# Performance work log

Measured on AMD Instinct MI355X. Metric: run time of the kernel, lower is better.

Reference implementation:

```python
import jax, jax.numpy as jnp
import numpy as np
from jax import lax

BN_EPS = 1e-5
K = 2  # kernel_size


def setup_inputs() -> dict:
    key = jax.random.key(0)
    k1, k2, k3 = jax.random.split(key, 3)
    x = jax.random.normal(k1, (64, 3, 256, 256), dtype=jnp.float32)
    conv_w = jax.random.normal(k2, (16, 3, K, K), dtype=jnp.float32) * 0.1
    conv_b = jax.random.normal(k3, (16,), dtype=jnp.float32) * 0.1
    gamma = jnp.ones((16,), dtype=jnp.float32)
    beta = jnp.zeros((16,), dtype=jnp.float32)
    return {"x": x, "conv_w": conv_w, "conv_b": conv_b, "gamma": gamma, "beta": beta}


def _forward(x, conv_w, conv_b, gamma, beta):
    # Conv2d, stride 1, VALID padding -> [B, C, H, W]
    feat = lax.conv_general_dilated(
        x, conv_w, window_strides=(1, 1), padding="VALID",
        dimension_numbers=("NCHW", "OIHW", "NCHW"))
    feat = feat + conv_b[None, :, None, None]
    # BatchNorm2d in training mode: batch stats over (B, H, W) per channel
    mu = jnp.mean(feat, axis=(0, 2, 3), keepdims=True)
    var = jnp.var(feat, axis=(0, 2, 3), keepdims=True)
    feat = (feat - mu) * lax.rsqrt(var + BN_EPS)
    feat = feat * gamma[None, :, None, None] + beta[None, :, None, None]
    feat = jax.nn.relu(feat)
    # Default quantum filter: mean(tanh(window)) over [C, k, k] window at every (b, i, j)
    t = jnp.tanh(feat)
    C = t.shape[1]
    win_sum = lax.reduce_window(
        t, jnp.float32(0), lax.add,
        window_dimensions=(1, C, K, K), window_strides=(1, 1, 1, 1),
        padding="VALID")  # [B, 1, H-k+1, W-k+1]
    out = win_sum / (C * K * K)
    # Flatten in (b, i, j) order, matching the triple loop
    return out.reshape(-1)


def reference(x, conv_w, conv_b, gamma, beta):
    return _forward(x, conv_w, conv_b, gamma, beta)
```

## Files before the change

kernel.cpp:

```cpp
#include <hip/hip_runtime.h>

#define B     64
#define CIN   3
#define COUT  16
#define H     256
#define W     256
#define HW    (H*W)
#define CHW   (CIN*H*W)
#define HO    255
#define WO    255
#define HF    254
#define WF    254
#define NPIXF 4161600.0f
#define BN_EPS 1e-5f
#define C2TANH 2.8853900817779268f

#define SEGS  32
#define NITEM (B * HO * SEGS)
#define STB   (NITEM / 256)

#define RB    7
#define RBLKS 37
#define LSTR  260

__device__ __forceinline__ float4 ld4(const float* p) { return *(const float4*)p; }

__device__ __forceinline__ void load_patch(const float* xp, int off8,
                                           float x0[CIN][9], float x1[CIN][9]) {
#pragma unroll
    for (int ic = 0; ic < CIN; ic++) {
        const float* p0 = xp + ic * HW;
        const float* p1 = p0 + W;
        float4 a = ld4(p0), b = ld4(p0 + 4);
        x0[ic][0] = a.x; x0[ic][1] = a.y; x0[ic][2] = a.z; x0[ic][3] = a.w;
        x0[ic][4] = b.x; x0[ic][5] = b.y; x0[ic][6] = b.z; x0[ic][7] = b.w;
        x0[ic][8] = p0[off8];
        float4 c4 = ld4(p1), d = ld4(p1 + 4);
        x1[ic][0] = c4.x; x1[ic][1] = c4.y; x1[ic][2] = c4.z; x1[ic][3] = c4.w;
        x1[ic][4] = d.x;  x1[ic][5] = d.y;  x1[ic][6] = d.z;  x1[ic][7] = d.w;
        x1[ic][8] = p1[off8];
    }
}

#define CONV_F(u)                                                  \
    float f = wd.x;                                                \
    f = fmaf(wa.x, x0[0][u], f); f = fmaf(wa.y, x0[0][(u)+1], f);  \
    f = fmaf(wa.z, x1[0][u], f); f = fmaf(wa.w, x1[0][(u)+1], f);  \
    f = fmaf(wb.x, x0[1][u], f); f = fmaf(wb.y, x0[1][(u)+1], f);  \
    f = fmaf(wb.z, x1[1][u], f); f = fmaf(wb.w, x1[1][(u)+1], f);  \
    f = fmaf(wc4.x, x0[2][u], f); f = fmaf(wc4.y, x0[2][(u)+1], f);\
    f = fmaf(wc4.z, x1[2][u], f); f = fmaf(wc4.w, x1[2][(u)+1], f);

__global__ __launch_bounds__(256) void k_stats(const float* __restrict__ x,
                                               const float* __restrict__ w,
                                               const float* __restrict__ bias,
                                               float* __restrict__ acc) {
    __shared__ float wpk[COUT * 16];
    int tid = threadIdx.x;
    {
        int c = tid >> 4, k = tid & 15;
        float v = 0.f;
        if (k < 12)       v = w[c * 12 + k];
        else if (k == 12) v = bias[c];
        wpk[tid] = v;
    }
    __syncthreads();

    int item = blockIdx.x * 256 + tid;
    int jseg = item & (SEGS - 1);
    int row  = item >> 5;
    int bb   = row / HO;
    int i    = row - bb * HO;
    const float* xp = x + (size_t)bb * CHW + i * W + (jseg << 3);
    bool tail = (jseg == SEGS - 1);
    int  off8 = tail ? 7 : 8;
    float m7  = tail ? 0.f : 1.f;

    float x0[CIN][9], x1[CIN][9];
    load_patch(xp, off8, x0, x1);

    float s[COUT], q[COUT];
#pragma unroll
    for (int c = 0; c < COUT; c++) {
        const float4* wv = (const float4*)(wpk + (c << 4));
        float4 wa = wv[0], wb = wv[1], wc4 = wv[2], wd = wv[3];
        float sc_ = 0.f, qc_ = 0.f;
#pragma unroll
        for (int u = 0; u < 8; u++) {
            CONV_F(u)
            if (u == 7) f *= m7;
            sc_ += f;
            qc_ = fmaf(f, f, qc_);
        }
        s[c] = sc_;
        q[c] = qc_;
    }

#pragma unroll
    for (int c = 0; c < COUT; c++) {
        for (int off = 32; off; off >>= 1) {
            s[c] += __shfl_down(s[c], off, 64);
            q[c] += __shfl_down(q[c], off, 64);
        }
    }
    __shared__ float red[4][2 * COUT];
    int wave = tid >> 6, lane = tid & 63;
    if (lane == 0) {
#pragma unroll
        for (int c = 0; c < COUT; c++) {
            red[wave][c] = s[c];
            red[wave][COUT + c] = q[c];
        }
    }
    __syncthreads();
    if (tid < 2 * COUT) {
        float v = red[0][tid] + red[1][tid] + red[2][tid] + red[3][tid];
        atomicAdd(&acc[tid], v);
    }
}

__global__ __launch_bounds__(256) void k_csum(const float* __restrict__ x,
                                              const float* __restrict__ w,
                                              const float* __restrict__ bias,
                                              const float* __restrict__ gamma,
                                              const float* __restrict__ beta,
                                              const float* __restrict__ acc,
                                              float* __restrict__ out) {
    __shared__ float wpk[COUT * 16];
    __shared__ float sld[(RB + 1) * LSTR];
    int tid = threadIdx.x;
    {
        int c = tid >> 4, k = tid & 15;
        float v = 0.f;
        if (k < 12)       v = w[c * 12 + k];
        else if (k == 12) v = bias[c];
        else if (k < 15) {
            float sv = acc[c], qv = acc[COUT + c];
            float mu  = sv * (1.f / NPIXF);
            float var = qv * (1.f / NPIXF) - mu * mu;
            float sc  = gamma[c] * rsqrtf(var + BN_EPS);
            v = (k == 13) ? sc * C2TANH : (beta[c] - mu * sc) * C2TANH;
        }
        wpk[tid] = v;
    }
    int blk   = blockIdx.x;
    int bb    = blk / RBLKS;
    int rblk  = blk - bb * RBLKS;
    int rbase = rblk * RB;
    __syncthreads();

    int sr = tid >> 5;
    int si = rbase + sr;
    int jseg = tid & 31;
    int j0 = jseg << 3;
    if (si < HO) {
        const float* xp = x + (size_t)bb * CHW + si * W + j0;
        int off8 = (jseg == 31) ? 7 : 8;
        float x0[CIN][9], x1[CIN][9];
        load_patch(xp, off8, x0, x1);

        float sum[8];
#pragma unroll
        for (int u = 0; u < 8; u++) sum[u] = 0.f;

#pragma unroll
        for (int c = 0; c < COUT; c++) {
            const float4* wv4 = (const float4*)(wpk + (c << 4));
            float4 wa = wv4[0], wb = wv4[1], wc4 = wv4[2], wd = wv4[3];
#pragma unroll
            for (int u = 0; u < 8; u++) {
                CONV_F(u)
                float a2 = fmaf(wd.y, f, wd.z);
                a2 = fmaxf(a2, 0.f);
                float E = __builtin_amdgcn_exp2f(a2);
                float r = __builtin_amdgcn_rcpf(E + 1.f);
                sum[u] += r;
            }
        }
        float* sp = &sld[sr * LSTR + j0];
        *(float4*)sp       = make_float4(fmaf(-2.f, sum[0], (float)COUT),
                                         fmaf(-2.f, sum[1], (float)COUT),
                                         fmaf(-2.f, sum[2], (float)COUT),
                                         fmaf(-2.f, sum[3], (float)COUT));
        *(float4*)(sp + 4) = make_float4(fmaf(-2.f, sum[4], (float)COUT),
                                         fmaf(-2.f, sum[5], (float)COUT),
                                         fmaf(-2.f, sum[6], (float)COUT),
                                         fmaf(-2.f, sum[7], (float)COUT));
    }
    __syncthreads();

    int orl = tid >> 5;
    int orow = rbase + orl;
    if (orl < RB && orow < HF) {
        const float* s0 = &sld[orl * LSTR];
        const float* s1 = s0 + LSTR;
        float* op = out + ((size_t)bb * HF + orow) * WF;
        int oc0 = tid & 31;
#pragma unroll
        for (int u = 0; u < 8; u++) {
            int c = oc0 + (u << 5);
            if (c < WF) {
                op[c] = (s0[c] + s0[c+1] + s1[c] + s1[c+1]) * (1.f / (COUT * 4));
            }
        }
    }
}

extern "C" void kernel_launch(void* const* d_in, const int* in_sizes, int n_in,
                              void* d_out, int out_size, void* d_ws, size_t ws_size,
                              hipStream_t stream) {
    const float* x     = (const float*)d_in[0];
    const float* w     = (const float*)d_in[1];
    const float* bias  = (const float*)d_in[2];
    const float* gamma = (const float*)d_in[3];
    const float* beta  = (const float*)d_in[4];
    float* out = (float*)d_out;

    float* acc = (float*)d_ws;

    hipMemsetAsync(d_ws, 0, 128, stream);
    k_stats<<<STB, 256, 0, stream>>>(x, w, bias, acc);
    k_csum<<<B * RBLKS, 256, 0, stream>>>(x, w, bias, gamma, beta, acc, out);
}
```

Measured before the change: 182.1 us.

## Replace atomic stats accumulation with per-block partials and a reduce kernel

k_stats now writes per-block sums into a partials buffer instead of doing global atomicAdds. The block reduction switches from wave shuffles to a transposed shared-memory reduction. A new single-block kernel sums the partials into the accumulator, which also removes the memset. This aims to cut atomic contention and shuffle cost, and makes the sum order deterministic. The trade-offs are an extra launch, a serial single-block reduce over about 4080 rows, and much more shared memory per block, which may lower occupancy.

```diff
diff --git a/kernel.cpp b/kernel.cpp
--- a/kernel.cpp
+++ b/kernel.cpp
@@ -18,6 +18,7 @@
 #define SEGS  32
 #define NITEM (B * HO * SEGS)
 #define STB   (NITEM / 256)
+#define RCHUNK (STB / 8)
 
 #define RB    7
 #define RBLKS 37
@@ -54,8 +55,10 @@
 __global__ __launch_bounds__(256) void k_stats(const float* __restrict__ x,
                                                const float* __restrict__ w,
                                                const float* __restrict__ bias,
-                                               float* __restrict__ acc) {
+                                               float* __restrict__ part) {
     __shared__ float wpk[COUT * 16];
+    __shared__ float tr[256 * 33];
+    __shared__ float red2[8 * 33];
     int tid = threadIdx.x;
     {
         int c = tid >> 4, k = tid & 15;
@@ -79,7 +82,6 @@
     float x0[CIN][9], x1[CIN][9];
     load_patch(xp, off8, x0, x1);
 
-    float s[COUT], q[COUT];
 #pragma unroll
     for (int c = 0; c < COUT; c++) {
         const float4* wv = (const float4*)(wpk + (c << 4));
@@ -92,30 +94,55 @@
             sc_ += f;
             qc_ = fmaf(f, f, qc_);
         }
-        s[c] = sc_;
-        q[c] = qc_;
-    }
-
-#pragma unroll
-    for (int c = 0; c < COUT; c++) {
-        for (int off = 32; off; off >>= 1) {
-            s[c] += __shfl_down(s[c], off, 64);
-            q[c] += __shfl_down(q[c], off, 64);
-        }
-    }
-    __shared__ float red[4][2 * COUT];
-    int wave = tid >> 6, lane = tid & 63;
-    if (lane == 0) {
-#pragma unroll
-        for (int c = 0; c < COUT; c++) {
-            red[wave][c] = s[c];
-            red[wave][COUT + c] = q[c];
-        }
-    }
-    __syncthreads();
-    if (tid < 2 * COUT) {
-        float v = red[0][tid] + red[1][tid] + red[2][tid] + red[3][tid];
-        atomicAdd(&acc[tid], v);
+        tr[tid * 33 + c]        = sc_;
+        tr[tid * 33 + COUT + c] = qc_;
+    }
+    __syncthreads();
+
+    {
+        int col = tid & 31, chunk = tid >> 5;
+        int r0 = chunk << 5;
+        float a0 = 0.f, a1 = 0.f, a2 = 0.f, a3 = 0.f;
+#pragma unroll
+        for (int k = 0; k < 32; k += 4) {
+            a0 += tr[(r0 + k)     * 33 + col];
+            a1 += tr[(r0 + k + 1) * 33 + col];
+            a2 += tr[(r0 + k + 2) * 33 + col];
+            a3 += tr[(r0 + k + 3) * 33 + col];
+        }
+        red2[chunk * 33 + col] = (a0 + a1) + (a2 + a3);
+    }
+    __syncthreads();
+    if (tid < 32) {
+        float s = 0.f;
+#pragma unroll
+        for (int k = 0; k < 8; k++) s += red2[k * 33 + tid];
+        part[blockIdx.x * 32 + tid] = s;
+    }
+}
+
+__global__ __launch_bounds__(256) void k_reduce(const float* __restrict__ part,
+                                                float* __restrict__ acc) {
+    __shared__ float red2[8 * 33];
+    int tid = threadIdx.x;
+    int col = tid & 31, chunk = tid >> 5;
+    int base = chunk * RCHUNK;
+    float a0 = 0.f, a1 = 0.f, a2 = 0.f, a3 = 0.f;
+    int k = 0;
+    for (; k + 3 < RCHUNK; k += 4) {
+        a0 += part[(base + k)     * 32 + col];
+        a1 += part[(base + k + 1) * 32 + col];
+        a2 += part[(base + k + 2) * 32 + col];
+        a3 += part[(base + k + 3) * 32 + col];
+    }
+    for (; k < RCHUNK; k++) a0 += part[(base + k) * 32 + col];
+    red2[chunk * 33 + col] = (a0 + a1) + (a2 + a3);
+    __syncthreads();
+    if (tid < 32) {
+        float s = 0.f;
+#pragma unroll
+        for (int j = 0; j < 8; j++) s += red2[j * 33 + tid];
+        acc[tid] = s;
     }
 }
 
@@ -216,9 +243,10 @@
     const float* beta  = (const float*)d_in[4];
     float* out = (float*)d_out;
 
-    float* acc = (float*)d_ws;
-
-    hipMemsetAsync(d_ws, 0, 128, stream);
-    k_stats<<<STB, 256, 0, stream>>>(x, w, bias, acc);
+    float* part = (float*)d_ws;
+    float* acc  = part + STB * 32;
+
+    k_stats<<<STB, 256, 0, stream>>>(x, w, bias, part);
+    k_reduce<<<1, 256, 0, stream>>>(part, acc);
     k_csum<<<B * RBLKS, 256, 0, stream>>>(x, w, bias, gamma, beta, acc, out);
 }
```

Result: faster. 154.8 us (-15.0%).
